# Performance work log

Hardware: AMD Instinct MI355X
Metric: run time of the kernel (lower is better)

Reference implementation:

```python
import jax, jax.numpy as jnp
import numpy as np

C = 1.0
SQRT_C = 1.0
EPS = 4e-3        # Poincare ball proj eps for float32
MIN_NORM = 1e-15
N_NODES = 50000
N_EDGES = 800000
NFEAT, NOUT, NHID, HEADS = 128, 64, 32, 4


def _norm(t):
    return jnp.clip(jnp.linalg.norm(t, axis=-1, keepdims=True), MIN_NORM)


def artanh(t):
    t = jnp.clip(t, -1.0 + 1e-7, 1.0 - 1e-7)
    return 0.5 * (jnp.log1p(t) - jnp.log1p(-t))


def proj(t):
    n = _norm(t)
    maxnorm = (1.0 - EPS) / SQRT_C
    return jnp.where(n > maxnorm, t / n * maxnorm, t)


def expmap0(u):
    n = _norm(u)
    return jnp.tanh(SQRT_C * n) * u / (SQRT_C * n)


def logmap0(p):
    n = _norm(p)
    return artanh(SQRT_C * n) * p / (SQRT_C * n)


def mobius_add(a, b):
    a2 = jnp.sum(a * a, -1, keepdims=True)
    b2 = jnp.sum(b * b, -1, keepdims=True)
    ab = jnp.sum(a * b, -1, keepdims=True)
    num = (1.0 + 2.0 * C * ab + C * b2) * a + (1.0 - C * a2) * b
    den = 1.0 + 2.0 * C * ab + C * C * a2 * b2
    return num / jnp.clip(den, MIN_NORM)


def mobius_matvec(W, t):
    mx = t @ W.T
    xn = _norm(t)
    mxn = _norm(mx)
    res = jnp.tanh(mxn / xn * artanh(SQRT_C * xn)) * mx / (mxn * SQRT_C)
    zero = jnp.all(mx == 0, axis=-1, keepdims=True)
    return jnp.where(zero, jnp.zeros_like(res), res)


def hyp_linear(t, W, b):
    res = proj(mobius_matvec(W, t))
    hyp_b = proj(expmap0(b[None, :]))  # proj_tan0 is identity on Poincare ball
    return proj(mobius_add(res, hyp_b))


def leaky_relu(t, slope):
    return jnp.where(t >= 0, t, slope * t)


def hyp_att_agg(h, src, dst, att_i, att_j, heads, concat):
    n = h.shape[0]
    d = h.shape[1] // heads
    ht = logmap0(h)                          # tangent space at origin
    x_i = ht[src].reshape(-1, heads, d)      # target (aggregation) endpoint
    x_j = ht[dst].reshape(-1, heads, d)      # source (message) endpoint
    alpha = (x_i * att_i).sum(-1) + (x_j * att_j).sum(-1)   # [E, heads]
    alpha = leaky_relu(alpha, 0.2)
    amax = jax.ops.segment_max(alpha, src, num_segments=n)
    e = jnp.exp(alpha - amax[src])
    denom = jax.ops.segment_sum(e, src, num_segments=n)
    alpha = e / (denom[src] + 1e-16)
    out = jax.ops.segment_sum(x_j * alpha[..., None], src, num_segments=n)  # [N,h,d]
    out = out.reshape(n, heads * d) if concat else out.mean(axis=1)
    return proj(expmap0(out))


def hyp_act(h, slope=0.01):
    return proj(expmap0(leaky_relu(logmap0(h), slope)))


def _glorot(key, shape):
    fan = shape[-1] + (shape[-2] if len(shape) > 1 else shape[-1])
    a = np.sqrt(6.0 / fan).astype(np.float32)
    return jax.random.uniform(key, shape, jnp.float32, -a, a)


def setup_inputs() -> dict:
    key = jax.random.key(0)
    ks = jax.random.split(key, 12)
    return {
        "x": jax.random.normal(ks[0], (N_NODES, NFEAT), jnp.float32),
        "Wl": _glorot(ks[1], (NOUT, NFEAT)),
        "bl": jnp.zeros((NOUT,), jnp.float32),
        "W1": _glorot(ks[2], (NHID * HEADS, NOUT)),
        "b1": jnp.zeros((NHID * HEADS,), jnp.float32),
        "ai1": _glorot(ks[3], (1, HEADS, NHID)),
        "aj1": _glorot(ks[4], (1, HEADS, NHID)),
        "W2": _glorot(ks[5], (NOUT * HEADS, NHID * HEADS)),
        "b2": jnp.zeros((NOUT * HEADS,), jnp.float32),
        "ai2": _glorot(ks[6], (1, HEADS, NOUT)),
        "aj2": _glorot(ks[7], (1, HEADS, NOUT)),
        "edge_index": jax.random.randint(ks[8], (2, N_EDGES), 0, N_NODES, jnp.int64 if jax.config.jax_enable_x64 else jnp.int32),
    }


def reference(x, Wl, bl, W1, b1, ai1, aj1, W2, b2, ai2, aj2, edge_index):
    n = x.shape[0]
    loops = jnp.arange(n, dtype=edge_index.dtype)
    ei = jnp.concatenate([edge_index, jnp.stack([loops, loops])], axis=1)
    src, dst = ei[0], ei[1]
    h = x @ Wl.T + bl                     # Euclidean linear
    h = proj(expmap0(h))                  # initHyperX (proj_tan0 = identity)
    h = proj(h)
    # layer1: HGATConv(nout -> nhid, heads, concat=True)
    h = hyp_linear(h, W1, b1)
    h = hyp_att_agg(h, src, dst, ai1, aj1, HEADS, True)
    h = hyp_act(h)
    h = proj(h)
    # layer2: HGATConv(nhid*heads -> nout, heads, concat=False)
    h = hyp_linear(h, W2, b2)
    h = hyp_att_agg(h, src, dst, ai2, aj2, HEADS, False)
    h = hyp_act(h)
    return logmap0(h)                     # toTangentX (proj_tan0 = identity)
```

## Files before the change

kernel.cpp:

```cpp
#include <hip/hip_runtime.h>
#include <hip/hip_fp16.h>

#define NN 50000
#define NER 800000
#define NE 850000
#define MAXN 0.996f
#define MINNRM 1e-15f
#define SCAN_B 256
#define NBLK ((NN + SCAN_B - 1) / SCAN_B)
#define HB ((NE + 255) / 256)
#define G0B ((NN + 63) / 64)

typedef _Float16 h2 __attribute__((ext_vector_type(2)));
typedef _Float16 h8 __attribute__((ext_vector_type(8)));
typedef float f32x4 __attribute__((ext_vector_type(4)));
union UB4 { uint4 u; h2 h[4]; };

__device__ __forceinline__ h2 f2h2(float a, float b){ h2 r; r.x=(_Float16)a; r.y=(_Float16)b; return r; }
__device__ __forceinline__ h2 splat(float a){ h2 r; r.x=(_Float16)a; r.y=(_Float16)a; return r; }

__device__ __forceinline__ float gsum16(float v){
  v += __shfl_xor(v, 1, 64); v += __shfl_xor(v, 2, 64);
  v += __shfl_xor(v, 4, 64); v += __shfl_xor(v, 8, 64);
  return v;
}
__device__ __forceinline__ float gmax16(float v){
  v = fmaxf(v, __shfl_xor(v, 1, 64)); v = fmaxf(v, __shfl_xor(v, 2, 64));
  v = fmaxf(v, __shfl_xor(v, 4, 64)); v = fmaxf(v, __shfl_xor(v, 8, 64));
  return v;
}
__device__ __forceinline__ float artanh_c(float t){
  t = fminf(t, 1.0f - 1e-7f);
  return 0.5f * (log1pf(t) - log1pf(-t));
}
__device__ __forceinline__ float lrelu(float t, float s){ return t >= 0.f ? t : s * t; }

__device__ void bias_blk(const float* b, const float* ai, const float* aj, int L, int HS, float* hbx){
  __shared__ float red[256];
  __shared__ float hai[4], haj[4];
  int t = threadIdx.x;
  float v = (t < L) ? b[t] : 0.f;
  red[t] = v * v; __syncthreads();
  for (int s = 128; s; s >>= 1){ if (t < s) red[t] += red[t + s]; __syncthreads(); }
  float n  = fmaxf(sqrtf(red[0]), MINNRM);
  float un = tanhf(n);
  float nn = un;
  float f  = un / n;
  if (un > MAXN){ f = MAXN / n; nn = MAXN; }
  float hb = v * f;
  if (t < L) hbx[t] = hb;
  if (t < 4){ hai[t] = 0.f; haj[t] = 0.f; }
  __syncthreads();
  if (t < L){
    int h = t / HS;
    atomicAdd(&hai[h], hb * ai[t]);
    atomicAdd(&haj[h], hb * aj[t]);
  }
  __syncthreads();
  if (t == 0) hbx[L] = nn * nn;
  if (t < 4){ hbx[L + 1 + t] = hai[t]; hbx[L + 5 + t] = haj[t]; }
}

__device__ __forceinline__ void wconv(const float* in, __half* outp, int Nr, int Kc, int i){
  int tot = Nr * (Kc >> 1);
  if (i >= tot) return;
  int kp = i / Nr, n = i % Nr;
  __half2 v;
  v.x = __float2half(in[(size_t)n * Kc + 2 * kp]);
  v.y = __float2half(in[(size_t)n * Kc + 2 * kp + 1]);
  ((__half2*)outp)[i] = v;
}

__global__ __launch_bounds__(256) void kprep(
    const float* __restrict__ b1, const float* __restrict__ ai1, const float* __restrict__ aj1, float* __restrict__ hbx1,
    const float* __restrict__ b2, const float* __restrict__ ai2, const float* __restrict__ aj2, float* __restrict__ hbx2,
    const float* __restrict__ Wl, __half* __restrict__ Wlh,
    const float* __restrict__ W1, __half* __restrict__ W1h,
    const float* __restrict__ W2, __half* __restrict__ W2m,
    const int* __restrict__ ei, int* __restrict__ cnt, int* __restrict__ rank){
  int bid = blockIdx.x, tid = threadIdx.x;
  if (bid == 0){ bias_blk(b1, ai1, aj1, 128, 32, hbx1); return; }
  if (bid == 1){ bias_blk(b2, ai2, aj2, 256, 64, hbx2); return; }
  if (bid < 18){ wconv(Wl, Wlh, 64, 128, (bid - 2) * 256 + tid); return; }
  if (bid < 34){ wconv(W1, W1h, 128, 64, (bid - 18) * 256 + tid); return; }
  if (bid < 162){
    int i = (bid - 34) * 256 + tid;
    if (i < 256 * 128) W2m[i] = __float2half(W2[i]);
    return;
  }
  int e = (bid - 162) * 256 + tid;
  if (e >= NE) return;
  int s = (e < NER) ? ei[e] : (e - NER);
  rank[e] = atomicAdd(&cnt[s], 1);
}

__device__ void kg0_body(int bid, const float* __restrict__ x, const __half* __restrict__ Wlh,
                         const float* __restrict__ bl, __half* __restrict__ h0h,
                         float* __restrict__ xn0){
  __shared__ __align__(16) h2 As2[16][68];
  __shared__ __align__(16) h2 Bs2[16][68];
  __shared__ float red[64][2];
  __shared__ float fsc[64];
  int tid = threadIdx.x, wave = tid >> 6, lane = tid & 63;
  int wr = wave >> 1, wc = wave & 1, lr = lane >> 3, lc = lane & 7;
  int row0 = bid * 64;
  int r0 = wr * 32 + lr * 4, c0 = wc * 32 + lc * 4;
  float acc[4][4] = {};
  int am = tid >> 2, aq = tid & 3;
  int bkp = tid >> 4, bn4 = (tid & 15) * 4;
  const uint* Wlu = (const uint*)Wlh;
  float4 ra0, ra1; uint4 rb;
  {
    int row = row0 + am;
    ra0 = make_float4(0.f,0.f,0.f,0.f); ra1 = ra0;
    if (row < NN){
      ra0 = *(const float4*)(x + (size_t)row * 128 + aq * 8);
      ra1 = *(const float4*)(x + (size_t)row * 128 + aq * 8 + 4);
    }
    rb = *(const uint4*)(Wlu + (size_t)bkp * 64 + bn4);
  }
  for (int ks = 0; ks < 4; ks++){
    __syncthreads();
    As2[aq*4+0][am] = f2h2(ra0.x, ra0.y);
    As2[aq*4+1][am] = f2h2(ra0.z, ra0.w);
    As2[aq*4+2][am] = f2h2(ra1.x, ra1.y);
    As2[aq*4+3][am] = f2h2(ra1.z, ra1.w);
    *(uint4*)&Bs2[bkp][bn4] = rb;
    __syncthreads();
    if (ks < 3){
      int k0 = (ks + 1) * 32;
      int row = row0 + am;
      ra0 = make_float4(0.f,0.f,0.f,0.f); ra1 = ra0;
      if (row < NN){
        ra0 = *(const float4*)(x + (size_t)row * 128 + k0 + aq * 8);
        ra1 = *(const float4*)(x + (size_t)row * 128 + k0 + aq * 8 + 4);
      }
      rb = *(const uint4*)(Wlu + (size_t)((ks + 1) * 16 + bkp) * 64 + bn4);
    }
#pragma unroll
    for (int kp = 0; kp < 16; kp++){
      UB4 av, bv;
      av.u = *(const uint4*)&As2[kp][r0];
      bv.u = *(const uint4*)&Bs2[kp][c0];
#pragma unroll
      for (int i = 0; i < 4; i++)
#pragma unroll
        for (int j = 0; j < 4; j++)
          acc[i][j] = __builtin_amdgcn_fdot2(av.h[i], bv.h[j], acc[i][j], false);
    }
  }
  float bb[4];
  *(float4*)&bb[0] = *(const float4*)(bl + c0);
#pragma unroll
  for (int i = 0; i < 4; i++){
    float rs = 0.f;
#pragma unroll
    for (int j = 0; j < 4; j++){ acc[i][j] += bb[j]; rs = fmaf(acc[i][j], acc[i][j], rs); }
    rs += __shfl_xor(rs, 1, 64);
    rs += __shfl_xor(rs, 2, 64);
    rs += __shfl_xor(rs, 4, 64);
    if (lc == 0) red[r0 + i][wc] = rs;
  }
  __syncthreads();
  if (tid < 64){
    int row = row0 + tid;
    if (row < NN){
      float rs = red[tid][0] + red[tid][1];
      float n  = fmaxf(sqrtf(rs), MINNRM);
      float un = tanhf(n);
      float f, nm;
      if (un > MAXN){ f = MAXN / n; nm = MAXN; } else { f = un / n; nm = un; }
      fsc[tid] = f;
      xn0[row] = nm;
    }
  }
  __syncthreads();
#pragma unroll
  for (int i = 0; i < 4; i++){
    int row = row0 + r0 + i;
    if (row >= NN) continue;
    float f = fsc[r0 + i];
    union { uint2 u; __half2 h[2]; } st;
    st.h[0] = __floats2half2_rn(acc[i][0] * f, acc[i][1] * f);
    st.h[1] = __floats2half2_rn(acc[i][2] * f, acc[i][3] * f);
    *(uint2*)(h0h + (size_t)row * 64 + c0) = st.u;
  }
}

__global__ __launch_bounds__(256) void kB(const int* __restrict__ cnt,
                                          int* __restrict__ part, int* __restrict__ bsum,
                                          const float* __restrict__ x, const __half* __restrict__ Wlh,
                                          const float* __restrict__ bl, __half* __restrict__ h0h,
                                          float* __restrict__ xn0){
  int bid = blockIdx.x;
  if (bid < NBLK){
    __shared__ int sh[SCAN_B];
    int t = threadIdx.x;
    int i = bid * SCAN_B + t;
    int v = (i < NN) ? cnt[i] : 0;
    sh[t] = v; __syncthreads();
    for (int d = 1; d < SCAN_B; d <<= 1){
      int u = (t >= d) ? sh[t - d] : 0;
      __syncthreads();
      sh[t] += u;
      __syncthreads();
    }
    if (i < NN) part[i] = sh[t];
    if (t == SCAN_B - 1) bsum[bid] = sh[t];
    return;
  }
  kg0_body(bid - NBLK, x, Wlh, bl, h0h, xn0);
}

__global__ __launch_bounds__(256) void kscan2(int* __restrict__ bsum){
  __shared__ int sh[256];
  int t = threadIdx.x;
  int v = (t < NBLK) ? bsum[t] : 0;
  sh[t] = v; __syncthreads();
  for (int d = 1; d < 256; d <<= 1){
    int u = (t >= d) ? sh[t - d] : 0;
    __syncthreads();
    sh[t] += u;
    __syncthreads();
  }
  if (t < NBLK) bsum[t] = sh[t];
}

__global__ __launch_bounds__(SCAN_B) void kscan3(const int* __restrict__ part, const int* __restrict__ bsum,
                                                 const int* __restrict__ cnt, int* __restrict__ rowptr){
  int t = threadIdx.x;
  int i = blockIdx.x * SCAN_B + t;
  if (i < NN){
    int base = blockIdx.x ? bsum[blockIdx.x - 1] : 0;
    rowptr[i] = base + part[i] - cnt[i];
  }
  if (i == 0) rowptr[NN] = bsum[NBLK - 1];
}

__device__ void kg1f_body(int bid, const __half* __restrict__ Ah, const __half* __restrict__ W1h,
    const float* __restrict__ xn0, const float* __restrict__ hbx,
    const float* __restrict__ ai, const float* __restrict__ aj,
    __half* __restrict__ ht1, float* __restrict__ s1i, float* __restrict__ s1j){
  __shared__ __align__(16) h2 As2[16][68];
  __shared__ __align__(16) h2 Bs2[16][132];
  __shared__ float red[64][12];
  __shared__ float pq1[64][4];
  int tid = threadIdx.x, wave = tid >> 6, lane = tid & 63;
  int wr = wave >> 1, wc = wave & 1, lr = lane >> 3, lc = lane & 7;
  int row0 = bid * 64;
  int r0 = wr * 32 + lr * 4, c0 = wc * 64 + lc * 8;
  float acc[4][8] = {};
  const uint* Au = (const uint*)Ah;
  const uint* Bu = (const uint*)W1h;
  int akp = tid & 15, am0 = (tid >> 4) * 4;
  int bkp = tid >> 4, bcol = (tid & 15) * 4;
  uint ua0, ua1, ua2, ua3; uint4 ub0, ub1;
  {
    int r;
    ua0 = ua1 = ua2 = ua3 = 0u;
    r = row0 + am0 + 0; if (r < NN) ua0 = Au[(size_t)r * 32 + akp];
    r = row0 + am0 + 1; if (r < NN) ua1 = Au[(size_t)r * 32 + akp];
    r = row0 + am0 + 2; if (r < NN) ua2 = Au[(size_t)r * 32 + akp];
    r = row0 + am0 + 3; if (r < NN) ua3 = Au[(size_t)r * 32 + akp];
    ub0 = *(const uint4*)(Bu + (size_t)bkp * 128 + bcol);
    ub1 = *(const uint4*)(Bu + (size_t)bkp * 128 + bcol + 64);
  }
  for (int ks = 0; ks < 2; ks++){
    __syncthreads();
    { uint4 av4; av4.x = ua0; av4.y = ua1; av4.z = ua2; av4.w = ua3;
      *(uint4*)&As2[akp][am0] = av4; }
    *(uint4*)&Bs2[bkp][bcol]      = ub0;
    *(uint4*)&Bs2[bkp][bcol + 64] = ub1;
    __syncthreads();
    if (ks < 1){
      int r;
      ua0 = ua1 = ua2 = ua3 = 0u;
      r = row0 + am0 + 0; if (r < NN) ua0 = Au[(size_t)r * 32 + 16 + akp];
      r = row0 + am0 + 1; if (r < NN) ua1 = Au[(size_t)r * 32 + 16 + akp];
      r = row0 + am0 + 2; if (r < NN) ua2 = Au[(size_t)r * 32 + 16 + akp];
      r = row0 + am0 + 3; if (r < NN) ua3 = Au[(size_t)r * 32 + 16 + akp];
      ub0 = *(const uint4*)(Bu + (size_t)(16 + bkp) * 128 + bcol);
      ub1 = *(const uint4*)(Bu + (size_t)(16 + bkp) * 128 + bcol + 64);
    }
#pragma unroll
    for (int kp = 0; kp < 16; kp++){
      UB4 av, bv0, bv1;
      av.u  = *(const uint4*)&As2[kp][r0];
      bv0.u = *(const uint4*)&Bs2[kp][c0];
      bv1.u = *(const uint4*)&Bs2[kp][c0 + 4];
#pragma unroll
      for (int i = 0; i < 4; i++){
#pragma unroll
        for (int j = 0; j < 4; j++)
          acc[i][j] = __builtin_amdgcn_fdot2(av.h[i], bv0.h[j], acc[i][j], false);
#pragma unroll
        for (int j = 4; j < 8; j++)
          acc[i][j] = __builtin_amdgcn_fdot2(av.h[i], bv1.h[j - 4], acc[i][j], false);
      }
    }
  }
  float hbv[8], aiv[8], ajv[8];
  *(float4*)&hbv[0] = *(const float4*)(hbx + c0); *(float4*)&hbv[4] = *(const float4*)(hbx + c0 + 4);
  *(float4*)&aiv[0] = *(const float4*)(ai + c0);  *(float4*)&aiv[4] = *(const float4*)(ai + c0 + 4);
  *(float4*)&ajv[0] = *(const float4*)(aj + c0);  *(float4*)&ajv[4] = *(const float4*)(aj + c0 + 4);
  int head = wc * 2 + (lc >> 2);
#pragma unroll
  for (int i = 0; i < 4; i++){
    float p1=0.f, p2=0.f, pai=0.f, paj=0.f;
#pragma unroll
    for (int j = 0; j < 8; j++){
      float a = acc[i][j];
      p1 += a*a; p2 += a*hbv[j]; pai += a*aiv[j]; paj += a*ajv[j];
    }
    p1 += __shfl_xor(p1,1,64); p1 += __shfl_xor(p1,2,64); p1 += __shfl_xor(p1,4,64);
    p2 += __shfl_xor(p2,1,64); p2 += __shfl_xor(p2,2,64); p2 += __shfl_xor(p2,4,64);
    pai += __shfl_xor(pai,1,64); pai += __shfl_xor(pai,2,64);
    paj += __shfl_xor(paj,1,64); paj += __shfl_xor(paj,2,64);
    int rloc = r0 + i;
    if (lc == 0){ red[rloc][wc] = p1; red[rloc][2+wc] = p2; }
    if ((lc & 3) == 0){ red[rloc][4+head] = pai; red[rloc][8+head] = paj; }
  }
  __syncthreads();
  if (tid < 64){
    int row = row0 + tid;
    if (row < NN){
      float b2 = hbx[128];
      float S1 = red[tid][0] + red[tid][1];
      float S2 = red[tid][2] + red[tid][3];
      float xn = fmaxf(xn0[row], MINNRM);
      float r_art = artanh_c(xn);
      float mxn = fmaxf(sqrtf(S1), MINNRM);
      float tn = tanhf(mxn / xn * r_art);
      float sc_ = tn / mxn;
      float rn = tn;
      if (rn > MAXN){ sc_ *= MAXN / rn; rn = MAXN; }
      float a2r = rn * rn;
      float ab = sc_ * S2;
      float co1 = 1.f + 2.f*ab + b2, co2 = 1.f - a2r;
      float den = fmaxf(1.f + 2.f*ab + a2r*b2, MINNRM);
      float P = co1 * sc_ / den, Q = co2 / den;
      float hn2 = P*P*S1 + 2.f*P*Q*S2 + Q*Q*b2;
      float hn = fmaxf(sqrtf(hn2), MINNRM);
      if (hn > MAXN){ float R = MAXN / hn; P *= R; Q *= R; hn = MAXN; }
      float lf = artanh_c(hn) / hn;
      pq1[tid][0] = P; pq1[tid][1] = Q; pq1[tid][2] = lf;
#pragma unroll
      for (int h = 0; h < 4; h++){
        s1i[row*4+h] = lf * (P * red[tid][4+h] + Q * hbx[129+h]);
        s1j[row*4+h] = lf * (P * red[tid][8+h] + Q * hbx[133+h]);
      }
    }
  }
  __syncthreads();
#pragma unroll
  for (int i = 0; i < 4; i++){
    int row = row0 + r0 + i;
    if (row >= NN) continue;
    int rloc = r0 + i;
    float P = pq1[rloc][0], Q = pq1[rloc][1], lf = pq1[rloc][2];
    union { __half h[8]; float4 f4; } ho;
#pragma unroll
    for (int j = 0; j < 8; j++) ho.h[j] = __float2half(lf * (P * acc[i][j] + Q * hbv[j]));
    *(float4*)(ht1 + (size_t)row * 128 + c0) = ho.f4;
  }
}

__global__ __launch_bounds__(256) void kE(const int* __restrict__ ei, const int* __restrict__ rowptr,
    const int* __restrict__ rank, int* __restrict__ col,
    const __half* __restrict__ Ah, const __half* __restrict__ W1h,
    const float* __restrict__ xn0, const float* __restrict__ hbx,
    const float* __restrict__ ai, const float* __restrict__ aj,
    __half* __restrict__ ht1, float* __restrict__ s1i, float* __restrict__ s1j){
  int bid = blockIdx.x;
  if (bid >= G0B){
    int e = (bid - G0B) * 256 + threadIdx.x;
    if (e >= NE) return;
    int s, d;
    if (e < NER){ s = ei[e]; d = ei[NER + e]; }
    else { s = e - NER; d = s; }
    col[rowptr[s] + rank[e]] = d;
    return;
  }
  kg1f_body(bid, Ah, W1h, xn0, hbx, ai, aj, ht1, s1i, s1j);
}

__global__ __launch_bounds__(256) void kg2m(const __half* __restrict__ Ah, const __half* __restrict__ W2m,
    const float* __restrict__ xn1, const float* __restrict__ hbx,
    const float* __restrict__ ai, const float* __restrict__ aj,
    __half* __restrict__ ht2, float* __restrict__ s2i, float* __restrict__ s2j){
  __shared__ float red[32][16];
  __shared__ float pqlf[32][4];
  int tid = threadIdx.x, w = tid >> 6, lane = tid & 63;
  int lm = lane & 15, lg = lane >> 4;
  int row0 = blockIdx.x * 32;
  const _Float16* Af = (const _Float16*)Ah;
  const _Float16* Bf = (const _Float16*)W2m;
  const _Float16* A0 = Af + (size_t)(row0 + lm) * 128 + lg * 8;
  h8 a00 = *(const h8*)(A0);
  h8 a01 = *(const h8*)(A0 + 32);
  h8 a02 = *(const h8*)(A0 + 64);
  h8 a03 = *(const h8*)(A0 + 96);
  h8 a10, a11, a12, a13;
  h8 zf = {};
  bool v1 = (row0 + 31) < NN;
  if (v1){
    const _Float16* A1 = Af + (size_t)(row0 + 16 + lm) * 128 + lg * 8;
    a10 = *(const h8*)(A1);
    a11 = *(const h8*)(A1 + 32);
    a12 = *(const h8*)(A1 + 64);
    a13 = *(const h8*)(A1 + 96);
  } else { a10 = zf; a11 = zf; a12 = zf; a13 = zf; }
  f32x4 c00 = {0.f,0.f,0.f,0.f}, c01 = c00, c02 = c00, c03 = c00;
  f32x4 c10 = c00, c11 = c00, c12 = c00, c13 = c00;
#define DO_CT(CT, C0, C1) { \
    const _Float16* Bp = Bf + (size_t)(w * 64 + (CT) * 16 + lm) * 128 + lg * 8; \
    h8 b0 = *(const h8*)(Bp); \
    h8 b1 = *(const h8*)(Bp + 32); \
    h8 b2v = *(const h8*)(Bp + 64); \
    h8 b3 = *(const h8*)(Bp + 96); \
    C0 = __builtin_amdgcn_mfma_f32_16x16x32_f16(a00, b0,  C0, 0, 0, 0); \
    C0 = __builtin_amdgcn_mfma_f32_16x16x32_f16(a01, b1,  C0, 0, 0, 0); \
    C0 = __builtin_amdgcn_mfma_f32_16x16x32_f16(a02, b2v, C0, 0, 0, 0); \
    C0 = __builtin_amdgcn_mfma_f32_16x16x32_f16(a03, b3,  C0, 0, 0, 0); \
    C1 = __builtin_amdgcn_mfma_f32_16x16x32_f16(a10, b0,  C1, 0, 0, 0); \
    C1 = __builtin_amdgcn_mfma_f32_16x16x32_f16(a11, b1,  C1, 0, 0, 0); \
    C1 = __builtin_amdgcn_mfma_f32_16x16x32_f16(a12, b2v, C1, 0, 0, 0); \
    C1 = __builtin_amdgcn_mfma_f32_16x16x32_f16(a13, b3,  C1, 0, 0, 0); }
  DO_CT(0, c00, c10)
  DO_CT(1, c01, c11)
  DO_CT(2, c02, c12)
  DO_CT(3, c03, c13)
#undef DO_CT
  int cb = w * 64 + lm;
  float hb0 = hbx[cb], hb1 = hbx[cb+16], hb2c = hbx[cb+32], hb3c = hbx[cb+48];
  float ai0 = ai[cb], ai1v = ai[cb+16], ai2c = ai[cb+32], ai3 = ai[cb+48];
  float aj0 = aj[cb], aj1v = aj[cb+16], aj2c = aj[cb+32], aj3 = aj[cb+48];
#pragma unroll
  for (int rt = 0; rt < 2; rt++){
#pragma unroll
    for (int ri = 0; ri < 4; ri++){
      float v0 = rt ? c10[ri] : c00[ri];
      float v1v = rt ? c11[ri] : c01[ri];
      float v2v = rt ? c12[ri] : c02[ri];
      float v3v = rt ? c13[ri] : c03[ri];
      float p1 = v0*v0 + v1v*v1v + v2v*v2v + v3v*v3v;
      float p2 = v0*hb0 + v1v*hb1 + v2v*hb2c + v3v*hb3c;
      float pa = v0*ai0 + v1v*ai1v + v2v*ai2c + v3v*ai3;
      float pj = v0*aj0 + v1v*aj1v + v2v*aj2c + v3v*aj3;
      p1 = gsum16(p1); p2 = gsum16(p2); pa = gsum16(pa); pj = gsum16(pj);
      if (lm == 0){
        int rloc = rt*16 + lg*4 + ri;
        red[rloc][w] = p1; red[rloc][4+w] = p2; red[rloc][8+w] = pa; red[rloc][12+w] = pj;
      }
    }
  }
  __syncthreads();
  if (tid < 32){
    int row = row0 + tid;
    if (row < NN){
      float b2s = hbx[256];
      float S1 = red[tid][0]+red[tid][1]+red[tid][2]+red[tid][3];
      float S2 = red[tid][4]+red[tid][5]+red[tid][6]+red[tid][7];
      float xn = fmaxf(xn1[row], MINNRM);
      float r_art = artanh_c(xn);
      float mxn = fmaxf(sqrtf(S1), MINNRM);
      float tn = tanhf(mxn / xn * r_art);
      float sc_ = tn / mxn;
      float rn = tn;
      if (rn > MAXN){ sc_ *= MAXN / rn; rn = MAXN; }
      float a2r = rn * rn;
      float ab = sc_ * S2;
      float co1 = 1.f + 2.f*ab + b2s, co2 = 1.f - a2r;
      float den = fmaxf(1.f + 2.f*ab + a2r*b2s, MINNRM);
      float P = co1 * sc_ / den, Q = co2 / den;
      float hn2 = P*P*S1 + 2.f*P*Q*S2 + Q*Q*b2s;
      float hn = fmaxf(sqrtf(hn2), MINNRM);
      if (hn > MAXN){ float R = MAXN / hn; P *= R; Q *= R; hn = MAXN; }
      float lf = artanh_c(hn) / hn;
      pqlf[tid][0] = P; pqlf[tid][1] = Q; pqlf[tid][2] = lf;
#pragma unroll
      for (int h = 0; h < 4; h++){
        s2i[row*4+h] = lf * (P * red[tid][8+h]  + Q * hbx[257+h]);
        s2j[row*4+h] = lf * (P * red[tid][12+h] + Q * hbx[261+h]);
      }
    }
  }
  __syncthreads();
#pragma unroll
  for (int rt = 0; rt < 2; rt++){
#pragma unroll
    for (int ri = 0; ri < 4; ri++){
      int row = row0 + rt*16 + lg*4 + ri;
      if (row >= NN) continue;
      int rloc = rt*16 + lg*4 + ri;
      float P = pqlf[rloc][0], Q = pqlf[rloc][1], lf = pqlf[rloc][2];
      float v0 = rt ? c10[ri] : c00[ri];
      float v1v = rt ? c11[ri] : c01[ri];
      float v2v = rt ? c12[ri] : c02[ri];
      float v3v = rt ? c13[ri] : c03[ri];
      __half* hp = ht2 + (size_t)row * 256 + w * 64 + lm;
      hp[0]  = __float2half(lf * (P * v0  + Q * hb0));
      hp[16] = __float2half(lf * (P * v1v + Q * hb1));
      hp[32] = __float2half(lf * (P * v2v + Q * hb2c));
      hp[48] = __float2half(lf * (P * v3v + Q * hb3c));
    }
  }
}

__global__ __launch_bounds__(256) void k_agg1(const int* __restrict__ rowptr, const int* __restrict__ col,
    const __half* __restrict__ ht1, const float* __restrict__ s1i, const float* __restrict__ s1j,
    __half* __restrict__ hacth, float* __restrict__ xn1){
  __shared__ int    sd[4][4][68];
  __shared__ float4 swl[4][4][66];
  int tid = threadIdx.x, wave = tid >> 6, lane = tid & 63;
  int g = lane >> 4, l = lane & 15, hh = l >> 2;
  int n = blockIdx.x * 16 + wave * 4 + g;
  int p0 = rowptr[n], p1 = rowptr[n + 1];
  float4 si = *(const float4*)(s1i + (size_t)n * 4);
  float m0=-1e30f,m1=-1e30f,m2=-1e30f,m3=-1e30f;
  float s0=0.f,s1=0.f,s2=0.f,s3=0.f;
  h2 acc2[4] = {};
  for (int base = p0; base < p1; base += 64){
    float a[4][4];
#pragma unroll
    for (int ss = 0; ss < 4; ss++){
      a[ss][0] = a[ss][1] = a[ss][2] = a[ss][3] = -1e30f;
      int e = base + ss * 16 + l;
      if (e < p1){
        int d = col[e];
        float4 sj = *(const float4*)(s1j + (size_t)d * 4);
        a[ss][0] = lrelu(si.x + sj.x, 0.2f);
        a[ss][1] = lrelu(si.y + sj.y, 0.2f);
        a[ss][2] = lrelu(si.z + sj.z, 0.2f);
        a[ss][3] = lrelu(si.w + sj.w, 0.2f);
        sd[wave][g][ss * 16 + l] = d;
      }
// ... 101 lines not shown
    for (int ss = 0; ss < 4; ss++){
      a[ss][0] = a[ss][1] = a[ss][2] = a[ss][3] = -1e30f;
      int e = base + ss * 16 + l;
      if (e < p1){
        int d = col[e];
        float4 sj = *(const float4*)(s2j + (size_t)d * 4);
        a[ss][0] = lrelu(si.x + sj.x, 0.2f);
        a[ss][1] = lrelu(si.y + sj.y, 0.2f);
        a[ss][2] = lrelu(si.z + sj.z, 0.2f);
        a[ss][3] = lrelu(si.w + sj.w, 0.2f);
        sd[wave][g][ss * 16 + l] = d;
      }
    }
    float c0 = fmaxf(fmaxf(a[0][0], a[1][0]), fmaxf(a[2][0], a[3][0]));
    float c1 = fmaxf(fmaxf(a[0][1], a[1][1]), fmaxf(a[2][1], a[3][1]));
    float c2 = fmaxf(fmaxf(a[0][2], a[1][2]), fmaxf(a[2][2], a[3][2]));
    float c3 = fmaxf(fmaxf(a[0][3], a[1][3]), fmaxf(a[2][3], a[3][3]));
    float nm0 = fmaxf(m0, gmax16(c0)), nm1 = fmaxf(m1, gmax16(c1));
    float nm2 = fmaxf(m2, gmax16(c2)), nm3 = fmaxf(m3, gmax16(c3));
    float r0_ = __expf(m0 - nm0), r1_ = __expf(m1 - nm1);
    float r2_ = __expf(m2 - nm2), r3_ = __expf(m3 - nm3);
    float t0 = 0.f, t1 = 0.f, t2 = 0.f, t3 = 0.f;
#pragma unroll
    for (int ss = 0; ss < 4; ss++){
      float w0 = __expf(a[ss][0] - nm0), w1 = __expf(a[ss][1] - nm1);
      float w2 = __expf(a[ss][2] - nm2), w3 = __expf(a[ss][3] - nm3);
      swl[wave][g][ss * 16 + l] = make_float4(w0, w1, w2, w3);
      t0 += w0; t1 += w1; t2 += w2; t3 += w3;
    }
    s0 = s0 * r0_ + gsum16(t0); s1 = s1 * r1_ + gsum16(t1);
    s2 = s2 * r2_ + gsum16(t2); s3 = s3 * r3_ + gsum16(t3);
    m0 = nm0; m1 = nm1; m2 = nm2; m3 = nm3;
    float rsel = (hh==0)?r0_:(hh==1)?r1_:(hh==2)?r2_:r3_;
    h2 rs2 = splat(rsel);
#pragma unroll
    for (int j = 0; j < 8; j++) acc2[j] = acc2[j] * rs2;
    __builtin_amdgcn_wave_barrier();
    int cnt_ = min(p1 - base, 64);
    int e = 0;
    for (; e + 3 < cnt_; e += 4){
      int dA = sd[wave][g][e],   dB = sd[wave][g][e+1];
      int dC = sd[wave][g][e+2], dD = sd[wave][g][e+3];
      h2 wA2 = splat(((const float*)&swl[wave][g][e])[hh]);
      h2 wB2 = splat(((const float*)&swl[wave][g][e+1])[hh]);
      h2 wC2 = splat(((const float*)&swl[wave][g][e+2])[hh]);
      h2 wD2 = splat(((const float*)&swl[wave][g][e+3])[hh]);
      const __half* pA = ht2 + (size_t)dA * 256 + 16*l;
      const __half* pB = ht2 + (size_t)dB * 256 + 16*l;
      const __half* pC = ht2 + (size_t)dC * 256 + 16*l;
      const __half* pD = ht2 + (size_t)dD * 256 + 16*l;
      UB4 uA0, uA1, uB0, uB1, uC0, uC1, uD0, uD1;
      uA0.u = *(const uint4*)pA; uA1.u = *(const uint4*)(pA + 8);
      uB0.u = *(const uint4*)pB; uB1.u = *(const uint4*)(pB + 8);
      uC0.u = *(const uint4*)pC; uC1.u = *(const uint4*)(pC + 8);
      uD0.u = *(const uint4*)pD; uD1.u = *(const uint4*)(pD + 8);
#pragma unroll
      for (int j = 0; j < 4; j++){
        acc2[j]   = acc2[j]   + wA2 * uA0.h[j] + wB2 * uB0.h[j] + wC2 * uC0.h[j] + wD2 * uD0.h[j];
        acc2[4+j] = acc2[4+j] + wA2 * uA1.h[j] + wB2 * uB1.h[j] + wC2 * uC1.h[j] + wD2 * uD1.h[j];
      }
    }
    for (; e < cnt_; e++){
      int dA = sd[wave][g][e];
      h2 wA2 = splat(((const float*)&swl[wave][g][e])[hh]);
      const __half* pA = ht2 + (size_t)dA * 256 + 16*l;
      UB4 uA0, uA1;
      uA0.u = *(const uint4*)pA; uA1.u = *(const uint4*)(pA + 8);
#pragma unroll
      for (int j = 0; j < 4; j++){
        acc2[j]   = acc2[j]   + wA2 * uA0.h[j];
        acc2[4+j] = acc2[4+j] + wA2 * uA1.h[j];
      }
    }
    __builtin_amdgcn_wave_barrier();
  }
  float ssel = (hh==0)?s0:(hh==1)?s1:(hh==2)?s2:s3;
  float rinv = 1.f / (ssel + 1e-16f);
  float accf[16];
#pragma unroll
  for (int j = 0; j < 4; j++){
    accf[2*j]     = (float)acc2[j].x;   accf[2*j+1]   = (float)acc2[j].y;
    accf[8+2*j]   = (float)acc2[4+j].x; accf[8+2*j+1] = (float)acc2[4+j].y;
  }
  float mj[16]; float sum2 = 0.f;
#pragma unroll
  for (int j = 0; j < 16; j++){
    float v = accf[j] * rinv;
    v += __shfl_xor(v, 4, 64);
    v += __shfl_xor(v, 8, 64);
    mj[j] = 0.25f * v;
    sum2 = fmaf(mj[j], mj[j], sum2);
  }
  sum2 = 0.25f * gsum16(sum2);
  float nn = fmaxf(sqrtf(sum2), MINNRM);
  float un = tanhf(nn);
  float f_, uN;
  if (un > MAXN){ f_ = MAXN / nn; uN = MAXN; } else { f_ = un / nn; uN = un; }
  float lg = artanh_c(uN) / fmaxf(uN, MINNRM);
  float tt[16]; float sum2b = 0.f;
#pragma unroll
  for (int j = 0; j < 16; j++){ tt[j] = lrelu(mj[j] * f_ * lg, 0.01f); sum2b = fmaf(tt[j], tt[j], sum2b); }
  sum2b = 0.25f * gsum16(sum2b);
  float nn2 = fmaxf(sqrtf(sum2b), MINNRM);
  float un2 = tanhf(nn2);
  float f2 = (un2 > MAXN) ? (MAXN / nn2) : (un2 / nn2);
  float uN2 = fminf(un2, MAXN);
  float lg2 = artanh_c(uN2) / fmaxf(uN2, MINNRM);
  if (hh == 0){
    float o[16];
#pragma unroll
    for (int j = 0; j < 16; j++) o[j] = tt[j] * f2 * lg2;
    float* op = out + (size_t)n * 64 + 16*l;
    *(float4*)op      = *(float4*)&o[0];
    *(float4*)(op+4)  = *(float4*)&o[4];
    *(float4*)(op+8)  = *(float4*)&o[8];
    *(float4*)(op+12) = *(float4*)&o[12];
  }
}

extern "C" void kernel_launch(void* const* d_in, const int* in_sizes, int n_in,
                              void* d_out, int out_size, void* d_ws, size_t ws_size,
                              hipStream_t stream){
  const float* x   = (const float*)d_in[0];
  const float* Wl  = (const float*)d_in[1];
  const float* bl  = (const float*)d_in[2];
  const float* W1  = (const float*)d_in[3];
  const float* b1  = (const float*)d_in[4];
  const float* ai1 = (const float*)d_in[5];
  const float* aj1 = (const float*)d_in[6];
  const float* W2  = (const float*)d_in[7];
  const float* b2  = (const float*)d_in[8];
  const float* ai2 = (const float*)d_in[9];
  const float* aj2 = (const float*)d_in[10];
  const int*   ei  = (const int*)d_in[11];
  float* out = (float*)d_out;
  float* ws  = (float*)d_ws;

  __half* h0h   = (__half*)(ws);
  __half* ht1h  = (__half*)(ws + 1600000);
  __half* hacth = (__half*)(ws + 4800000);
  __half* ht2h  = (__half*)(ws + 8000000);
  float* xn0    = ws + 14400000;
  float* xn1    = ws + 14450000;
  float* s1i    = ws + 14500000;
  float* s1j    = ws + 14700000;
  float* hbx1   = ws + 14900000;
  float* hbx2   = ws + 14900144;
  int* rowptr   = (int*)(ws + 14900416);
  int* cnt      = rowptr + NN + 1;
  int* col      = cnt + NN;
  int* part     = col + NE;
  int* bsum     = part + NN;
  int* rank     = bsum + NBLK;
  __half* Wlh   = (__half*)(ws + 16800000);
  __half* W1h   = (__half*)(ws + 16810000);
  __half* W2m   = (__half*)(ws + 16820000);

  hipMemsetAsync(cnt, 0, NN * sizeof(int), stream);
  kprep<<<162 + HB, 256, 0, stream>>>(b1, ai1, aj1, hbx1, b2, ai2, aj2, hbx2,
                                      Wl, Wlh, W1, W1h, W2, W2m, ei, cnt, rank);
  kB<<<NBLK + G0B, 256, 0, stream>>>(cnt, part, bsum, x, Wlh, bl, h0h, xn0);
  kscan2<<<1, 256, 0, stream>>>(bsum);
  kscan3<<<NBLK, SCAN_B, 0, stream>>>(part, bsum, cnt, rowptr);
  kE<<<G0B + HB, 256, 0, stream>>>(ei, rowptr, rank, col, h0h, W1h, xn0, hbx1, ai1, aj1, ht1h, s1i, s1j);
  k_agg1<<<NN / 16, 256, 0, stream>>>(rowptr, col, ht1h, s1i, s1j, hacth, xn1);
  kg2m<<<(NN + 31) / 32, 256, 0, stream>>>(hacth, W2m, xn1, hbx2, ai2, aj2, ht2h, s1i, s1j);
  k_agg2<<<NN / 16, 256, 0, stream>>>(rowptr, col, ht2h, s1i, s1j, out);
}
```

Baseline: 222.3 us.

## Replace fdot2 LDS-tiled GEMMs with direct-load MFMA 16x16x32 in first two layers

The Euclidean input linear and the first hyperbolic linear GEMMs now use MFMA f16 16x16x32 instructions instead of shared-memory tiles with packed fdot2. Operands load straight from global memory into registers, and the weights are stored row-major in half precision rather than repacked. This removes the LDS staging and barriers and moves the multiply-accumulate onto the matrix cores. The epilogue reductions now use 16-lane shuffles, and outputs go out as scattered 2-byte stores, which may coalesce worse than the earlier vector stores.

Result: no change. 226.5 us (+1.9%).

```diff
diff --git a/kernel.cpp b/kernel.cpp
--- a/kernel.cpp
+++ b/kernel.cpp
@@ -16,8 +16,15 @@
 typedef float f32x4 __attribute__((ext_vector_type(4)));
 union UB4 { uint4 u; h2 h[4]; };
 
-__device__ __forceinline__ h2 f2h2(float a, float b){ h2 r; r.x=(_Float16)a; r.y=(_Float16)b; return r; }
 __device__ __forceinline__ h2 splat(float a){ h2 r; r.x=(_Float16)a; r.y=(_Float16)a; return r; }
+
+__device__ __forceinline__ h8 cvt8(const float* p){
+  float4 f0 = *(const float4*)p, f1 = *(const float4*)(p + 4);
+  h8 r;
+  r[0]=(_Float16)f0.x; r[1]=(_Float16)f0.y; r[2]=(_Float16)f0.z; r[3]=(_Float16)f0.w;
+  r[4]=(_Float16)f1.x; r[5]=(_Float16)f1.y; r[6]=(_Float16)f1.z; r[7]=(_Float16)f1.w;
+  return r;
+}
 
 __device__ __forceinline__ float gsum16(float v){
   v += __shfl_xor(v, 1, 64); v += __shfl_xor(v, 2, 64);
@@ -61,111 +68,67 @@
   if (t < 4){ hbx[L + 1 + t] = hai[t]; hbx[L + 5 + t] = haj[t]; }
 }
 
-__device__ __forceinline__ void wconv(const float* in, __half* outp, int Nr, int Kc, int i){
-  int tot = Nr * (Kc >> 1);
-  if (i >= tot) return;
-  int kp = i / Nr, n = i % Nr;
-  __half2 v;
-  v.x = __float2half(in[(size_t)n * Kc + 2 * kp]);
-  v.y = __float2half(in[(size_t)n * Kc + 2 * kp + 1]);
-  ((__half2*)outp)[i] = v;
-}
-
 __global__ __launch_bounds__(256) void kprep(
     const float* __restrict__ b1, const float* __restrict__ ai1, const float* __restrict__ aj1, float* __restrict__ hbx1,
     const float* __restrict__ b2, const float* __restrict__ ai2, const float* __restrict__ aj2, float* __restrict__ hbx2,
-    const float* __restrict__ Wl, __half* __restrict__ Wlh,
-    const float* __restrict__ W1, __half* __restrict__ W1h,
+    const float* __restrict__ Wl, __half* __restrict__ Wlm,
+    const float* __restrict__ W1, __half* __restrict__ W1m,
     const float* __restrict__ W2, __half* __restrict__ W2m,
     const int* __restrict__ ei, int* __restrict__ cnt, int* __restrict__ rank){
   int bid = blockIdx.x, tid = threadIdx.x;
   if (bid == 0){ bias_blk(b1, ai1, aj1, 128, 32, hbx1); return; }
   if (bid == 1){ bias_blk(b2, ai2, aj2, 256, 64, hbx2); return; }
-  if (bid < 18){ wconv(Wl, Wlh, 64, 128, (bid - 2) * 256 + tid); return; }
-  if (bid < 34){ wconv(W1, W1h, 128, 64, (bid - 18) * 256 + tid); return; }
-  if (bid < 162){
-    int i = (bid - 34) * 256 + tid;
-    if (i < 256 * 128) W2m[i] = __float2half(W2[i]);
-    return;
-  }
-  int e = (bid - 162) * 256 + tid;
+  if (bid < 34){ int i = (bid - 2) * 256 + tid; if (i < 64*128) Wlm[i] = __float2half(Wl[i]); return; }
+  if (bid < 66){ int i = (bid - 34) * 256 + tid; if (i < 128*64) W1m[i] = __float2half(W1[i]); return; }
+  if (bid < 194){ int i = (bid - 66) * 256 + tid; if (i < 256*128) W2m[i] = __float2half(W2[i]); return; }
+  int e = (bid - 194) * 256 + tid;
   if (e >= NE) return;
   int s = (e < NER) ? ei[e] : (e - NER);
   rank[e] = atomicAdd(&cnt[s], 1);
 }
 
-__device__ void kg0_body(int bid, const float* __restrict__ x, const __half* __restrict__ Wlh,
+__device__ void kg0_body(int bid, const float* __restrict__ x, const __half* __restrict__ Wlm,
                          const float* __restrict__ bl, __half* __restrict__ h0h,
                          float* __restrict__ xn0){
-  __shared__ __align__(16) h2 As2[16][68];
-  __shared__ __align__(16) h2 Bs2[16][68];
-  __shared__ float red[64][2];
+  __shared__ float red[64];
   __shared__ float fsc[64];
-  int tid = threadIdx.x, wave = tid >> 6, lane = tid & 63;
-  int wr = wave >> 1, wc = wave & 1, lr = lane >> 3, lc = lane & 7;
+  int tid = threadIdx.x, w = tid >> 6, lane = tid & 63;
+  int lm = lane & 15, lg = lane >> 4;
   int row0 = bid * 64;
-  int r0 = wr * 32 + lr * 4, c0 = wc * 32 + lc * 4;
-  float acc[4][4] = {};
-  int am = tid >> 2, aq = tid & 3;
-  int bkp = tid >> 4, bn4 = (tid & 15) * 4;
-  const uint* Wlu = (const uint*)Wlh;
-  float4 ra0, ra1; uint4 rb;
-  {
-    int row = row0 + am;
-    ra0 = make_float4(0.f,0.f,0.f,0.f); ra1 = ra0;
-    if (row < NN){
-      ra0 = *(const float4*)(x + (size_t)row * 128 + aq * 8);
-      ra1 = *(const float4*)(x + (size_t)row * 128 + aq * 8 + 4);
-    }
-    rb = *(const uint4*)(Wlu + (size_t)bkp * 64 + bn4);
-  }
-  for (int ks = 0; ks < 4; ks++){
-    __syncthreads();
-    As2[aq*4+0][am] = f2h2(ra0.x, ra0.y);
-    As2[aq*4+1][am] = f2h2(ra0.z, ra0.w);
-    As2[aq*4+2][am] = f2h2(ra1.x, ra1.y);
-    As2[aq*4+3][am] = f2h2(ra1.z, ra1.w);
-    *(uint4*)&Bs2[bkp][bn4] = rb;
-    __syncthreads();
-    if (ks < 3){
-      int k0 = (ks + 1) * 32;
-      int row = row0 + am;
-      ra0 = make_float4(0.f,0.f,0.f,0.f); ra1 = ra0;
-      if (row < NN){
-        ra0 = *(const float4*)(x + (size_t)row * 128 + k0 + aq * 8);
-        ra1 = *(const float4*)(x + (size_t)row * 128 + k0 + aq * 8 + 4);
-      }
-      rb = *(const uint4*)(Wlu + (size_t)((ks + 1) * 16 + bkp) * 64 + bn4);
-    }
-#pragma unroll
-    for (int kp = 0; kp < 16; kp++){
-      UB4 av, bv;
-      av.u = *(const uint4*)&As2[kp][r0];
-      bv.u = *(const uint4*)&Bs2[kp][c0];
-#pragma unroll
-      for (int i = 0; i < 4; i++)
-#pragma unroll
-        for (int j = 0; j < 4; j++)
-          acc[i][j] = __builtin_amdgcn_fdot2(av.h[i], bv.h[j], acc[i][j], false);
-    }
-  }
-  float bb[4];
-  *(float4*)&bb[0] = *(const float4*)(bl + c0);
-#pragma unroll
-  for (int i = 0; i < 4; i++){
-    float rs = 0.f;
-#pragma unroll
-    for (int j = 0; j < 4; j++){ acc[i][j] += bb[j]; rs = fmaf(acc[i][j], acc[i][j], rs); }
-    rs += __shfl_xor(rs, 1, 64);
-    rs += __shfl_xor(rs, 2, 64);
-    rs += __shfl_xor(rs, 4, 64);
-    if (lc == 0) red[r0 + i][wc] = rs;
+  int arow = row0 + w * 16 + lm;
+  const _Float16* Bf = (const _Float16*)Wlm;
+  h8 a0 = {}, a1 = {}, a2 = {}, a3 = {};
+  if (arow < NN){
+    const float* xp = x + (size_t)arow * 128 + lg * 8;
+    a0 = cvt8(xp); a1 = cvt8(xp + 32); a2 = cvt8(xp + 64); a3 = cvt8(xp + 96);
+  }
+  f32x4 c0 = {0.f,0.f,0.f,0.f}, c1 = c0, c2 = c0, c3 = c0;
+#define G0_CT(CT, CC) { \
+    const _Float16* Bp = Bf + (size_t)((CT) * 16 + lm) * 128 + lg * 8; \
+    h8 b0 = *(const h8*)(Bp); h8 b1 = *(const h8*)(Bp + 32); \
+    h8 b2v = *(const h8*)(Bp + 64); h8 b3 = *(const h8*)(Bp + 96); \
+    CC = __builtin_amdgcn_mfma_f32_16x16x32_f16(a0, b0,  CC, 0, 0, 0); \
+    CC = __builtin_amdgcn_mfma_f32_16x16x32_f16(a1, b1,  CC, 0, 0, 0); \
+    CC = __builtin_amdgcn_mfma_f32_16x16x32_f16(a2, b2v, CC, 0, 0, 0); \
+    CC = __builtin_amdgcn_mfma_f32_16x16x32_f16(a3, b3,  CC, 0, 0, 0); }
+  G0_CT(0, c0)
+  G0_CT(1, c1)
+  G0_CT(2, c2)
+  G0_CT(3, c3)
+#undef G0_CT
+  float bl0 = bl[lm], bl1 = bl[16 + lm], bl2 = bl[32 + lm], bl3 = bl[48 + lm];
+#pragma unroll
+  for (int ri = 0; ri < 4; ri++){
+    float v0 = c0[ri] + bl0, v1 = c1[ri] + bl1, v2 = c2[ri] + bl2, v3 = c3[ri] + bl3;
+    float rs = v0*v0 + v1*v1 + v2*v2 + v3*v3;
+    rs = gsum16(rs);
+    if (lm == 0) red[w*16 + lg*4 + ri] = rs;
   }
   __syncthreads();
   if (tid < 64){
     int row = row0 + tid;
     if (row < NN){
-      float rs = red[tid][0] + red[tid][1];
+      float rs = red[tid];
       float n  = fmaxf(sqrtf(rs), MINNRM);
       float un = tanhf(n);
       float f, nm;
@@ -176,20 +139,21 @@
   }
   __syncthreads();
 #pragma unroll
-  for (int i = 0; i < 4; i++){
-    int row = row0 + r0 + i;
+  for (int ri = 0; ri < 4; ri++){
+    int row = row0 + w*16 + lg*4 + ri;
     if (row >= NN) continue;
-    float f = fsc[r0 + i];
-    union { uint2 u; __half2 h[2]; } st;
-    st.h[0] = __floats2half2_rn(acc[i][0] * f, acc[i][1] * f);
-    st.h[1] = __floats2half2_rn(acc[i][2] * f, acc[i][3] * f);
-    *(uint2*)(h0h + (size_t)row * 64 + c0) = st.u;
+    float f = fsc[w*16 + lg*4 + ri];
+    __half* hp = h0h + (size_t)row * 64 + lm;
+    hp[0]  = __float2half((c0[ri] + bl0) * f);
+    hp[16] = __float2half((c1[ri] + bl1) * f);
+    hp[32] = __float2half((c2[ri] + bl2) * f);
+    hp[48] = __float2half((c3[ri] + bl3) * f);
   }
 }
 
 __global__ __launch_bounds__(256) void kB(const int* __restrict__ cnt,
                                           int* __restrict__ part, int* __restrict__ bsum,
-                                          const float* __restrict__ x, const __half* __restrict__ Wlh,
+                                          const float* __restrict__ x, const __half* __restrict__ Wlm,
                                           const float* __restrict__ bl, __half* __restrict__ h0h,
                                           float* __restrict__ xn0){
   int bid = blockIdx.x;
@@ -209,7 +173,7 @@
     if (t == SCAN_B - 1) bsum[bid] = sh[t];
     return;
   }
-  kg0_body(bid - NBLK, x, Wlh, bl, h0h, xn0);
+  kg0_body(bid - NBLK, x, Wlm, bl, h0h, xn0);
 }
 
 __global__ __launch_bounds__(256) void kscan2(int* __restrict__ bsum){
@@ -237,96 +201,75 @@
   if (i == 0) rowptr[NN] = bsum[NBLK - 1];
 }
 
-__device__ void kg1f_body(int bid, const __half* __restrict__ Ah, const __half* __restrict__ W1h,
+__device__ void kg1f_body(int bid, const __half* __restrict__ Ah, const __half* __restrict__ W1m,
     const float* __restrict__ xn0, const float* __restrict__ hbx,
     const float* __restrict__ ai, const float* __restrict__ aj,
     __half* __restrict__ ht1, float* __restrict__ s1i, float* __restrict__ s1j){
-  __shared__ __align__(16) h2 As2[16][68];
-  __shared__ __align__(16) h2 Bs2[16][132];
-  __shared__ float red[64][12];
-  __shared__ float pq1[64][4];
-  int tid = threadIdx.x, wave = tid >> 6, lane = tid & 63;
-  int wr = wave >> 1, wc = wave & 1, lr = lane >> 3, lc = lane & 7;
+  __shared__ float red[64][10];
+  __shared__ float pq1[64][3];
+  int tid = threadIdx.x, w = tid >> 6, lane = tid & 63;
+  int lm = lane & 15, lg = lane >> 4;
   int row0 = bid * 64;
-  int r0 = wr * 32 + lr * 4, c0 = wc * 64 + lc * 8;
-  float acc[4][8] = {};
-  const uint* Au = (const uint*)Ah;
-  const uint* Bu = (const uint*)W1h;
-  int akp = tid & 15, am0 = (tid >> 4) * 4;
-  int bkp = tid >> 4, bcol = (tid & 15) * 4;
-  uint ua0, ua1, ua2, ua3; uint4 ub0, ub1;
-  {
-    int r;
-    ua0 = ua1 = ua2 = ua3 = 0u;
-    r = row0 + am0 + 0; if (r < NN) ua0 = Au[(size_t)r * 32 + akp];
-    r = row0 + am0 + 1; if (r < NN) ua1 = Au[(size_t)r * 32 + akp];
-    r = row0 + am0 + 2; if (r < NN) ua2 = Au[(size_t)r * 32 + akp];
-    r = row0 + am0 + 3; if (r < NN) ua3 = Au[(size_t)r * 32 + akp];
-    ub0 = *(const uint4*)(Bu + (size_t)bkp * 128 + bcol);
-    ub1 = *(const uint4*)(Bu + (size_t)bkp * 128 + bcol + 64);
-  }
-  for (int ks = 0; ks < 2; ks++){
-    __syncthreads();
-    { uint4 av4; av4.x = ua0; av4.y = ua1; av4.z = ua2; av4.w = ua3;
-      *(uint4*)&As2[akp][am0] = av4; }
-    *(uint4*)&Bs2[bkp][bcol]      = ub0;
-    *(uint4*)&Bs2[bkp][bcol + 64] = ub1;
-    __syncthreads();
-    if (ks < 1){
-      int r;
-      ua0 = ua1 = ua2 = ua3 = 0u;
-      r = row0 + am0 + 0; if (r < NN) ua0 = Au[(size_t)r * 32 + 16 + akp];
-      r = row0 + am0 + 1; if (r < NN) ua1 = Au[(size_t)r * 32 + 16 + akp];
-      r = row0 + am0 + 2; if (r < NN) ua2 = Au[(size_t)r * 32 + 16 + akp];
-      r = row0 + am0 + 3; if (r < NN) ua3 = Au[(size_t)r * 32 + 16 + akp];
-      ub0 = *(const uint4*)(Bu + (size_t)(16 + bkp) * 128 + bcol);
-      ub1 = *(const uint4*)(Bu + (size_t)(16 + bkp) * 128 + bcol + 64);
-    }
-#pragma unroll
-    for (int kp = 0; kp < 16; kp++){
-      UB4 av, bv0, bv1;
-      av.u  = *(const uint4*)&As2[kp][r0];
-      bv0.u = *(const uint4*)&Bs2[kp][c0];
-      bv1.u = *(const uint4*)&Bs2[kp][c0 + 4];
-#pragma unroll
-      for (int i = 0; i < 4; i++){
-#pragma unroll
-        for (int j = 0; j < 4; j++)
-          acc[i][j] = __builtin_amdgcn_fdot2(av.h[i], bv0.h[j], acc[i][j], false);
-#pragma unroll
-        for (int j = 4; j < 8; j++)
-          acc[i][j] = __builtin_amdgcn_fdot2(av.h[i], bv1.h[j - 4], acc[i][j], false);
-      }
-    }
-  }
-  float hbv[8], aiv[8], ajv[8];
-  *(float4*)&hbv[0] = *(const float4*)(hbx + c0); *(float4*)&hbv[4] = *(const float4*)(hbx + c0 + 4);
-  *(float4*)&aiv[0] = *(const float4*)(ai + c0);  *(float4*)&aiv[4] = *(const float4*)(ai + c0 + 4);
-  *(float4*)&ajv[0] = *(const float4*)(aj + c0);  *(float4*)&ajv[4] = *(const float4*)(aj + c0 + 4);
-  int head = wc * 2 + (lc >> 2);
-#pragma unroll
-  for (int i = 0; i < 4; i++){
-    float p1=0.f, p2=0.f, pai=0.f, paj=0.f;
-#pragma unroll
-    for (int j = 0; j < 8; j++){
-      float a = acc[i][j];
-      p1 += a*a; p2 += a*hbv[j]; pai += a*aiv[j]; paj += a*ajv[j];
-    }
-    p1 += __shfl_xor(p1,1,64); p1 += __shfl_xor(p1,2,64); p1 += __shfl_xor(p1,4,64);
-    p2 += __shfl_xor(p2,1,64); p2 += __shfl_xor(p2,2,64); p2 += __shfl_xor(p2,4,64);
-    pai += __shfl_xor(pai,1,64); pai += __shfl_xor(pai,2,64);
-    paj += __shfl_xor(paj,1,64); paj += __shfl_xor(paj,2,64);
-    int rloc = r0 + i;
-    if (lc == 0){ red[rloc][wc] = p1; red[rloc][2+wc] = p2; }
-    if ((lc & 3) == 0){ red[rloc][4+head] = pai; red[rloc][8+head] = paj; }
+  int arow = row0 + w * 16 + lm;
+  h8 a0 = {}, a1 = {};
+  if (arow < NN){
+    const _Float16* Ap = (const _Float16*)Ah + (size_t)arow * 64 + lg * 8;
+    a0 = *(const h8*)(Ap);
+    a1 = *(const h8*)(Ap + 32);
+  }
+  const _Float16* Bf = (const _Float16*)W1m;
+  f32x4 c0 = {0.f,0.f,0.f,0.f}, c1 = c0, c2 = c0, c3 = c0, c4 = c0, c5 = c0, c6 = c0, c7 = c0;
+#define G1_CT(CT, CC) { \
+    const _Float16* Bp = Bf + (size_t)((CT) * 16 + lm) * 64 + lg * 8; \
+    h8 b0 = *(const h8*)(Bp); h8 b1 = *(const h8*)(Bp + 32); \
+    CC = __builtin_amdgcn_mfma_f32_16x16x32_f16(a0, b0, CC, 0, 0, 0); \
+    CC = __builtin_amdgcn_mfma_f32_16x16x32_f16(a1, b1, CC, 0, 0, 0); }
+  G1_CT(0, c0)
+  G1_CT(1, c1)
+  G1_CT(2, c2)
+  G1_CT(3, c3)
+  G1_CT(4, c4)
+  G1_CT(5, c5)
+  G1_CT(6, c6)
+  G1_CT(7, c7)
+#undef G1_CT
+  float hb0 = hbx[lm],      hb1 = hbx[16+lm],  hb2 = hbx[32+lm],  hb3 = hbx[48+lm];
+  float hb4 = hbx[64+lm],   hb5 = hbx[80+lm],  hb6 = hbx[96+lm],  hb7 = hbx[112+lm];
+  float ai0 = ai[lm],  ai1v = ai[16+lm], ai2v = ai[32+lm], ai3v = ai[48+lm];
+  float ai4v = ai[64+lm], ai5v = ai[80+lm], ai6v = ai[96+lm], ai7v = ai[112+lm];
+  float aj0 = aj[lm],  aj1v = aj[16+lm], aj2v = aj[32+lm], aj3v = aj[48+lm];
+  float aj4v = aj[64+lm], aj5v = aj[80+lm], aj6v = aj[96+lm], aj7v = aj[112+lm];
+#pragma unroll
+  for (int ri = 0; ri < 4; ri++){
+    float v0 = c0[ri], v1 = c1[ri], v2 = c2[ri], v3 = c3[ri];
+    float v4 = c4[ri], v5 = c5[ri], v6 = c6[ri], v7 = c7[ri];
+    float p1 = v0*v0+v1*v1+v2*v2+v3*v3+v4*v4+v5*v5+v6*v6+v7*v7;
+    float p2 = v0*hb0+v1*hb1+v2*hb2+v3*hb3+v4*hb4+v5*hb5+v6*hb6+v7*hb7;
+    float pa0 = v0*ai0 + v1*ai1v;
+    float pa1 = v2*ai2v + v3*ai3v;
+    float pa2 = v4*ai4v + v5*ai5v;
+    float pa3 = v6*ai6v + v7*ai7v;
+    float pj0 = v0*aj0 + v1*aj1v;
+    float pj1 = v2*aj2v + v3*aj3v;
+    float pj2 = v4*aj4v + v5*aj5v;
+    float pj3 = v6*aj6v + v7*aj7v;
+    p1 = gsum16(p1); p2 = gsum16(p2);
+    pa0 = gsum16(pa0); pa1 = gsum16(pa1); pa2 = gsum16(pa2); pa3 = gsum16(pa3);
+    pj0 = gsum16(pj0); pj1 = gsum16(pj1); pj2 = gsum16(pj2); pj3 = gsum16(pj3);
+    if (lm == 0){
+      int rl = w*16 + lg*4 + ri;
+      red[rl][0] = p1; red[rl][1] = p2;
+      red[rl][2] = pa0; red[rl][3] = pa1; red[rl][4] = pa2; red[rl][5] = pa3;
+      red[rl][6] = pj0; red[rl][7] = pj1; red[rl][8] = pj2; red[rl][9] = pj3;
+    }
   }
   __syncthreads();
   if (tid < 64){
     int row = row0 + tid;
     if (row < NN){
       float b2 = hbx[128];
-      float S1 = red[tid][0] + red[tid][1];
-      float S2 = red[tid][2] + red[tid][3];
+      float S1 = red[tid][0];
+      float S2 = red[tid][1];
       float xn = fmaxf(xn0[row], MINNRM);
       float r_art = artanh_c(xn);
       float mxn = fmaxf(sqrtf(S1), MINNRM);
@@ -346,28 +289,33 @@
       pq1[tid][0] = P; pq1[tid][1] = Q; pq1[tid][2] = lf;
 #pragma unroll
       for (int h = 0; h < 4; h++){
-        s1i[row*4+h] = lf * (P * red[tid][4+h] + Q * hbx[129+h]);
-        s1j[row*4+h] = lf * (P * red[tid][8+h] + Q * hbx[133+h]);
+        s1i[row*4+h] = lf * (P * red[tid][2+h] + Q * hbx[129+h]);
+        s1j[row*4+h] = lf * (P * red[tid][6+h] + Q * hbx[133+h]);
       }
     }
   }
   __syncthreads();
 #pragma unroll
-  for (int i = 0; i < 4; i++){
-    int row = row0 + r0 + i;
+  for (int ri = 0; ri < 4; ri++){
+    int row = row0 + w*16 + lg*4 + ri;
     if (row >= NN) continue;
-    int rloc = r0 + i;
-    float P = pq1[rloc][0], Q = pq1[rloc][1], lf = pq1[rloc][2];
-    union { __half h[8]; float4 f4; } ho;
-#pragma unroll
-    for (int j = 0; j < 8; j++) ho.h[j] = __float2half(lf * (P * acc[i][j] + Q * hbv[j]));
-    *(float4*)(ht1 + (size_t)row * 128 + c0) = ho.f4;
+    int rl = w*16 + lg*4 + ri;
+    float P = pq1[rl][0], Q = pq1[rl][1], lf = pq1[rl][2];
+    __half* hp = ht1 + (size_t)row * 128 + lm;
+    hp[0]   = __float2half(lf * (P * c0[ri] + Q * hb0));
+    hp[16]  = __float2half(lf * (P * c1[ri] + Q * hb1));
+    hp[32]  = __float2half(lf * (P * c2[ri] + Q * hb2));
+    hp[48]  = __float2half(lf * (P * c3[ri] + Q * hb3));
+    hp[64]  = __float2half(lf * (P * c4[ri] + Q * hb4));
+    hp[80]  = __float2half(lf * (P * c5[ri] + Q * hb5));
+    hp[96]  = __float2half(lf * (P * c6[ri] + Q * hb6));
+    hp[112] = __float2half(lf * (P * c7[ri] + Q * hb7));
   }
 }
 
 __global__ __launch_bounds__(256) void kE(const int* __restrict__ ei, const int* __restrict__ rowptr,
     const int* __restrict__ rank, int* __restrict__ col,
-    const __half* __restrict__ Ah, const __half* __restrict__ W1h,
+    const __half* __restrict__ Ah, const __half* __restrict__ W1m,
     const float* __restrict__ xn0, const float* __restrict__ hbx,
     const float* __restrict__ ai, const float* __restrict__ aj,
     __half* __restrict__ ht1, float* __restrict__ s1i, float* __restrict__ s1j){
@@ -381,7 +329,7 @@
     col[rowptr[s] + rank[e]] = d;
     return;
   }
-  kg1f_body(bid, Ah, W1h, xn0, hbx, ai, aj, ht1, s1i, s1j);
+  kg1f_body(bid, Ah, W1m, xn0, hbx, ai, aj, ht1, s1i, s1j);
 }
 
 __global__ __launch_bounds__(256) void kg2m(const __half* __restrict__ Ah, const __half* __restrict__ W2m,
@@ -789,17 +737,17 @@
   int* part     = col + NE;
   int* bsum     = part + NN;
   int* rank     = bsum + NBLK;
-  __half* Wlh   = (__half*)(ws + 16800000);
-  __half* W1h   = (__half*)(ws + 16810000);
+  __half* Wlm   = (__half*)(ws + 16800000);
+  __half* W1m   = (__half*)(ws + 16810000);
   __half* W2m   = (__half*)(ws + 16820000);
 
   hipMemsetAsync(cnt, 0, NN * sizeof(int), stream);
-  kprep<<<162 + HB, 256, 0, stream>>>(b1, ai1, aj1, hbx1, b2, ai2, aj2, hbx2,
-                                      Wl, Wlh, W1, W1h, W2, W2m, ei, cnt, rank);
-  kB<<<NBLK + G0B, 256, 0, stream>>>(cnt, part, bsum, x, Wlh, bl, h0h, xn0);
+  kprep<<<194 + HB, 256, 0, stream>>>(b1, ai1, aj1, hbx1, b2, ai2, aj2, hbx2,
+                                      Wl, Wlm, W1, W1m, W2, W2m, ei, cnt, rank);
+  kB<<<NBLK + G0B, 256, 0, stream>>>(cnt, part, bsum, x, Wlm, bl, h0h, xn0);
   kscan2<<<1, 256, 0, stream>>>(bsum);
   kscan3<<<NBLK, SCAN_B, 0, stream>>>(part, bsum, cnt, rowptr);
-  kE<<<G0B + HB, 256, 0, stream>>>(ei, rowptr, rank, col, h0h, W1h, xn0, hbx1, ai1, aj1, ht1h, s1i, s1j);
+  kE<<<G0B + HB, 256, 0, stream>>>(ei, rowptr, rank, col, h0h, W1m, xn0, hbx1, ai1, aj1, ht1h, s1i, s1j);
   k_agg1<<<NN / 16, 256, 0, stream>>>(rowptr, col, ht1h, s1i, s1j, hacth, xn1);
   kg2m<<<(NN + 31) / 32, 256, 0, stream>>>(hacth, W2m, xn1, hbx2, ai2, aj2, ht2h, s1i, s1j);
   k_agg2<<<NN / 16, 256, 0, stream>>>(rowptr, col, ht2h, s1i, s1j, out);
```
